# Performance work log

Measured on AMD Instinct MI355X. Metric: run time of the kernel, lower is better.

The kernel has to match this reference:

```python
import jax, jax.numpy as jnp
import numpy as np

VAR_W = 1.0
DIST_W = 1.0
M_VAR = 0.1
M_DIST = 1.5
IGNORE = 255
C = 16  # static upper bound on instance ids (labels 1..C; 0 = background)


def setup_inputs() -> dict:
    key = jax.random.key(0)
    ks = jax.random.split(key, 6)
    shapes = [(16, 1, 1024, 1024), (16, 1, 512, 512), (16, 1, 256, 256)]
    d = {}
    for idx, s in enumerate(shapes):
        d[f"featmap{idx}"] = jax.random.normal(ks[idx], s, dtype=jnp.float32)
        d[f"gt{idx}"] = jax.random.randint(ks[3 + idx], s, 0, C + 1, dtype=jnp.int32)
    return d


def _push_pull(feats, gts):
    B = feats[0].shape[0]
    nseg = B * (C + 1)
    b_off = (jnp.arange(B, dtype=jnp.int32) * (C + 1))[:, None]  # [B,1]

    segs, valids, ffs = [], [], []
    tot_sum = jnp.zeros((nseg,), dtype=feats[0].dtype)
    tot_cnt = jnp.zeros((nseg,), dtype=feats[0].dtype)
    # pass 1: per (batch, instance) sums / counts pooled over all scales
    for f, g in zip(feats, gts):
        ff = f.reshape(B, -1)            # [B, N_s]
        gg = g.reshape(B, -1)
        valid = (gg >= 1) & (gg <= C) & (gg < IGNORE)
        lab = jnp.where(valid, gg, 0)
        seg = (lab + b_off).reshape(-1)  # [B*N_s], segment id = b*(C+1)+label
        vf = valid.reshape(-1).astype(ff.dtype)
        tot_sum = tot_sum + jax.ops.segment_sum(jnp.where(valid, ff, 0.0).reshape(-1), seg, num_segments=nseg)
        tot_cnt = tot_cnt + jax.ops.segment_sum(vf, seg, num_segments=nseg)
        segs.append(seg); valids.append(valid); ffs.append(ff)

    mean = tot_sum / jnp.maximum(tot_cnt, 1.0)  # [nseg] per-(b,instance) mean over all scales

    # pass 2: pull loss -- per-scale mean of clamp(|x - mean| - margin_var, 0)^2, summed over scales
    pull_seg = jnp.zeros((nseg,), dtype=feats[0].dtype)
    for ff, seg, valid in zip(ffs, segs, valids):
        m_pix = mean[seg].reshape(ff.shape)
        val = jnp.where(valid, jnp.square(jnp.maximum(jnp.abs(ff - m_pix) - M_VAR, 0.0)), 0.0)
        ssum = jax.ops.segment_sum(val.reshape(-1), seg, num_segments=nseg)
        scnt = jax.ops.segment_sum(valid.reshape(-1).astype(ff.dtype), seg, num_segments=nseg)
        pull_seg = pull_seg + jnp.where(scnt > 0, ssum / jnp.maximum(scnt, 1.0), 0.0)

    present = tot_cnt.reshape(B, C + 1)[:, 1:] > 0        # [B,C]
    pull_i = pull_seg.reshape(B, C + 1)[:, 1:]            # [B,C]
    n_pull = jnp.maximum(present.sum(), 1).astype(pull_i.dtype)
    pull_loss = jnp.sum(jnp.where(present, pull_i, 0.0)) / n_pull * VAR_W

    # push loss: all ordered pairs (i,j), i!=j, both present in that batch element
    m = mean.reshape(B, C + 1)[:, 1:]                     # [B,C]
    diff = jnp.abs(m[:, :, None] - m[:, None, :])         # [B,C,C]
    pv = jnp.square(jnp.maximum(2.0 * M_DIST - diff, 0.0))
    pm = present[:, :, None] & present[:, None, :] & ~jnp.eye(C, dtype=bool)[None]
    n_push = jnp.maximum(pm.sum(), 1).astype(pv.dtype)
    push_loss = jnp.sum(jnp.where(pm, pv, 0.0)) / n_push * DIST_W

    return push_loss + pull_loss


def reference(featmap0, featmap1, featmap2, gt0, gt1, gt2):
    return _push_pull([featmap0, featmap1, featmap2], [gt0, gt1, gt2])
```

## Files before the change

kernel.cpp:

```cpp
#include <hip/hip_runtime.h>


#define M_VAR 0.1f
#define TWO_M_DIST 3.0f

#define SUB0 64
#define SUB1 16
#define SUB2 4
#define PER_BATCH (SUB0 + SUB1 + SUB2)
#define NBATCH 16
#define GRID_BLOCKS (NBATCH * PER_BATCH)
#define NITER 16

#define OFF_PSUM  0
#define OFF_PCNT  (GRID_BLOCKS * 16)
#define OFF_MI    (2 * GRID_BLOCKS * 16)
#define OFF_GMEAN (OFF_MI + 3 * 16 * 17 * 2)
#define OFF_GCNT  (OFF_GMEAN + 256)
#define OFF_PULL  (OFF_GCNT + 256)
#define OFF_PLAB  46592
#define PLAB_BASE1 (16 * 262144)
#define PLAB_BASE2 (PLAB_BASE1 + 16 * 65536)
#define PLAB_TOTAL (PLAB_BASE2 + 16 * 16384)
#define WS_NEEDED ((size_t)(OFF_PLAB + PLAB_TOTAL) * 4)

struct Sel {
  const float4* f; const int4* g;
  int vbase, stride, batch, j, pbase;
};

__device__ __forceinline__ Sel pick(
    int bid, int t,
    const float4* f0, const int4* g0,
    const float4* f1, const int4* g1,
    const float4* f2, const int4* g2) {
  Sel s;
  s.batch = bid / PER_BATCH;
  s.j = bid - s.batch * PER_BATCH;
  if (s.j < SUB0) {
    s.f = f0; s.g = g0; s.pbase = 0;
    s.vbase = s.batch * 262144 + s.j * 256 + t;             s.stride = SUB0 * 256;
  } else if (s.j < SUB0 + SUB1) {
    s.f = f1; s.g = g1; s.pbase = PLAB_BASE1; int sub = s.j - SUB0;
    s.vbase = s.batch * 65536 + sub * 256 + t;              s.stride = SUB1 * 256;
  } else {
    s.f = f2; s.g = g2; s.pbase = PLAB_BASE2; int sub = s.j - SUB0 - SUB1;
    s.vbase = s.batch * 16384 + sub * 256 + t;              s.stride = SUB2 * 256;
  }
  return s;
}

template <bool PACKED>
__global__ __launch_bounds__(256, 4) void hist_kernel(
    const float4* __restrict__ f0, const int4* __restrict__ g0,
    const float4* __restrict__ f1, const int4* __restrict__ g1,
    const float4* __restrict__ f2, const int4* __restrict__ g2,
    float* __restrict__ ws, unsigned* __restrict__ plab)
{
  const int t = threadIdx.x, bid = blockIdx.x;
  Sel s = pick(bid, t, f0, g0, f1, g1, f2, g2);

  float sum[16];
  int   cnt[16];
  #pragma unroll
  for (int l = 0; l < 16; ++l) { sum[l] = 0.f; cnt[l] = 0; }

  int v = s.vbase;
  float4 fA = s.f[v];            int4 gA = s.g[v];
  float4 fB = s.f[v + s.stride]; int4 gB = s.g[v + s.stride];

  #pragma unroll 1
  for (int it = 0; it < NITER; ++it) {
    int vp = (it + 2 < NITER) ? (v + 2 * s.stride) : v;
    float4 fC = s.f[vp];
    int4   gC = s.g[vp];

    #pragma unroll
    for (int l = 0; l < 16; ++l) {
      bool cx = (gA.x == l + 1); sum[l] += cx ? fA.x : 0.f; cnt[l] += cx;
      bool cy = (gA.y == l + 1); sum[l] += cy ? fA.y : 0.f; cnt[l] += cy;
      bool cz = (gA.z == l + 1); sum[l] += cz ? fA.z : 0.f; cnt[l] += cz;
      bool cw = (gA.w == l + 1); sum[l] += cw ? fA.w : 0.f; cnt[l] += cw;
    }
    if (PACKED) {
      unsigned lx = min((unsigned)gA.x, 16u), ly = min((unsigned)gA.y, 16u);
      unsigned lz = min((unsigned)gA.z, 16u), lw = min((unsigned)gA.w, 16u);
      plab[s.pbase + v] = lx | (ly << 8) | (lz << 16) | (lw << 24);
    }

    fA = fB; gA = gB; fB = fC; gB = gC;
    v += s.stride;
  }

  __shared__ float rs[4][16];
  __shared__ float rc[4][16];
  const int lane = t & 63, wave = t >> 6;
  #pragma unroll
  for (int l = 0; l < 16; ++l) {
    float sv = sum[l];
    float cv = (float)cnt[l];
    #pragma unroll
    for (int o = 32; o > 0; o >>= 1) {
      sv += __shfl_down(sv, o);
      cv += __shfl_down(cv, o);
    }
    if (lane == 0) { rs[wave][l] = sv; rc[wave][l] = cv; }
  }
  __syncthreads();
  if (t < 16) {
    ws[OFF_PSUM + bid * 16 + t] = rs[0][t] + rs[1][t] + rs[2][t] + rs[3][t];
    ws[OFF_PCNT + bid * 16 + t] = rc[0][t] + rc[1][t] + rc[2][t] + rc[3][t];
  }
}

__global__ __launch_bounds__(256) void mean_kernel(float* __restrict__ ws) {
  const int b = blockIdx.x;
  const int t = threadIdx.x;
  const int label = t & 15, k = t >> 4;

  float ts = 0.f, tc = 0.f, c0 = 0.f, c1 = 0.f, c2 = 0.f;
  for (int jj = k; jj < PER_BATCH; jj += 16) {
    float sv = ws[OFF_PSUM + (b * PER_BATCH + jj) * 16 + label];
    float cv = ws[OFF_PCNT + (b * PER_BATCH + jj) * 16 + label];
    ts += sv; tc += cv;
    if (jj < SUB0) c0 += cv; else if (jj < SUB0 + SUB1) c1 += cv; else c2 += cv;
  }
  __shared__ float L[5][16][16];
  L[0][k][label] = ts; L[1][k][label] = tc;
  L[2][k][label] = c0; L[3][k][label] = c1; L[4][k][label] = c2;
  __syncthreads();

  float2* mi = (float2*)(ws + OFF_MI);
  if (t < 16) {
    float Ts = 0.f, Tc = 0.f, C0 = 0.f, C1 = 0.f, C2 = 0.f;
    #pragma unroll 1
    for (int kk = 0; kk < 16; ++kk) {
      Ts += L[0][kk][t]; Tc += L[1][kk][t];
      C0 += L[2][kk][t]; C1 += L[3][kk][t]; C2 += L[4][kk][t];
    }
    float mean = Ts / fmaxf(Tc, 1.f);
    ws[OFF_GMEAN + b * 16 + t] = mean;
    ws[OFF_GCNT  + b * 16 + t] = Tc;
    mi[(0 * 16 + b) * 17 + 1 + t] = make_float2(mean, (C0 > 0.f) ? (1.f / C0) : 0.f);
    mi[(1 * 16 + b) * 17 + 1 + t] = make_float2(mean, (C1 > 0.f) ? (1.f / C1) : 0.f);
    mi[(2 * 16 + b) * 17 + 1 + t] = make_float2(mean, (C2 > 0.f) ? (1.f / C2) : 0.f);
  } else if (t == 16) {
    mi[(0 * 16 + b) * 17] = make_float2(0.f, 0.f);
    mi[(1 * 16 + b) * 17] = make_float2(0.f, 0.f);
    mi[(2 * 16 + b) * 17] = make_float2(0.f, 0.f);
  }
}

template <bool PACKED>
__global__ __launch_bounds__(256, 8) void pull_kernel(
    const float4* __restrict__ f0, const int4* __restrict__ g0,
    const float4* __restrict__ f1, const int4* __restrict__ g1,
    const float4* __restrict__ f2, const int4* __restrict__ g2,
    float* __restrict__ ws, const unsigned* __restrict__ plab)
{
  const int t = threadIdx.x, bid = blockIdx.x;
  Sel s = pick(bid, t, f0, g0, f1, g1, f2, g2);
  const int myscale = (s.j < SUB0) ? 0 : ((s.j < SUB0 + SUB1) ? 1 : 2);

  __shared__ float2 s_mi[17];
  if (t < 17) s_mi[t] = ((const float2*)(ws + OFF_MI))[(myscale * 16 + s.batch) * 17 + t];
  __syncthreads();

  float acc = 0.f;
  int v = s.vbase;
  if (PACKED) {
    float4  fA = s.f[v];               unsigned pA = plab[s.pbase + v];
    float4  fB = s.f[v + s.stride];    unsigned pB = plab[s.pbase + v + s.stride];
    #pragma unroll 1
    for (int it = 0; it < NITER; ++it) {
      int vp = (it + 2 < NITER) ? (v + 2 * s.stride) : v;
      float4  fC = s.f[vp];
      unsigned pC = plab[s.pbase + vp];
      {
        float2 a = s_mi[pA & 255u];
        float d = fmaxf(fabsf(fA.x - a.x) - M_VAR, 0.f); acc += d * d * a.y;
      }
      {
        float2 a = s_mi[(pA >> 8) & 255u];
        float d = fmaxf(fabsf(fA.y - a.x) - M_VAR, 0.f); acc += d * d * a.y;
      }
      {
        float2 a = s_mi[(pA >> 16) & 255u];
        float d = fmaxf(fabsf(fA.z - a.x) - M_VAR, 0.f); acc += d * d * a.y;
      }
      {
        float2 a = s_mi[pA >> 24];
        float d = fmaxf(fabsf(fA.w - a.x) - M_VAR, 0.f); acc += d * d * a.y;
      }
      fA = fB; pA = pB; fB = fC; pB = pC;
      v += s.stride;
    }
  } else {
    float4 fA = s.f[v];            int4 gA = s.g[v];
    float4 fB = s.f[v + s.stride]; int4 gB = s.g[v + s.stride];
    #pragma unroll 1
    for (int it = 0; it < NITER; ++it) {
      int vp = (it + 2 < NITER) ? (v + 2 * s.stride) : v;
      float4 fC = s.f[vp];
      int4   gC = s.g[vp];
      {
        float2 a = s_mi[min((unsigned)gA.x, 16u)];
        float d = fmaxf(fabsf(fA.x - a.x) - M_VAR, 0.f); acc += d * d * a.y;
      }
      {
        float2 a = s_mi[min((unsigned)gA.y, 16u)];
        float d = fmaxf(fabsf(fA.y - a.x) - M_VAR, 0.f); acc += d * d * a.y;
      }
      {
        float2 a = s_mi[min((unsigned)gA.z, 16u)];
        float d = fmaxf(fabsf(fA.z - a.x) - M_VAR, 0.f); acc += d * d * a.y;
      }
      {
        float2 a = s_mi[min((unsigned)gA.w, 16u)];
        float d = fmaxf(fabsf(fA.w - a.x) - M_VAR, 0.f); acc += d * d * a.y;
      }
      fA = fB; gA = gB; fB = fC; gB = gC;
      v += s.stride;
    }
  }

  #pragma unroll
  for (int o = 32; o > 0; o >>= 1) acc += __shfl_down(acc, o);
  __shared__ float racc[4];
  if ((t & 63) == 0) racc[t >> 6] = acc;
  __syncthreads();
  if (t == 0) ws[OFF_PULL + bid] = racc[0] + racc[1] + racc[2] + racc[3];
}

__global__ __launch_bounds__(256) void finalize_kernel(
    const float* __restrict__ ws, float* __restrict__ out)
{
  const int t = threadIdx.x;
  __shared__ float s_mean[256];
  __shared__ float s_pres[256];
  {
    float cval = ws[OFF_GCNT + t];
    s_mean[t] = ws[OFF_GMEAN + t];
    s_pres[t] = (cval > 0.f) ? 1.f : 0.f;
  }
  __syncthreads();

  float pull_v = 0.f;
  for (int i = t; i < GRID_BLOCKS; i += 256) pull_v += ws[OFF_PULL + i];

  float pull_n = s_pres[t];
  float push_v = 0.f, push_n = 0.f;
  {
    int b = t >> 4, ii = t & 15;
    if (s_pres[t] > 0.f) {
      float mi = s_mean[t];
      for (int jj = 0; jj < 16; ++jj) {
        if (jj == ii) continue;
        int sj = (b << 4) | jj;
        if (s_pres[sj] > 0.f) {
          float d = fmaxf(TWO_M_DIST - fabsf(mi - s_mean[sj]), 0.f);
          push_v += d * d; push_n += 1.f;
        }
      }
    }
  }

  #pragma unroll
  for (int o = 32; o > 0; o >>= 1) {
    pull_v += __shfl_down(pull_v, o);
    pull_n += __shfl_down(pull_n, o);
    push_v += __shfl_down(push_v, o);
    push_n += __shfl_down(push_n, o);
  }
  __shared__ float r[4][4];
  int wave = t >> 6;
  if ((t & 63) == 0) { r[wave][0] = pull_v; r[wave][1] = pull_n; r[wave][2] = push_v; r[wave][3] = push_n; }
  __syncthreads();
  if (t == 0) {
    float PV = 0, PN = 0, SV = 0, SN = 0;
    for (int w = 0; w < 4; ++w) { PV += r[w][0]; PN += r[w][1]; SV += r[w][2]; SN += r[w][3]; }
    out[0] = PV / fmaxf(PN, 1.f) + SV / fmaxf(SN, 1.f);
  }
}

extern "C" void kernel_launch(void* const* d_in, const int* in_sizes, int n_in,
                              void* d_out, int out_size, void* d_ws, size_t ws_size,
                              hipStream_t stream) {
  const float4* f0 = (const float4*)d_in[0];
  const int4*   g0 = (const int4*)  d_in[1];
  const float4* f1 = (const float4*)d_in[2];
  const int4*   g1 = (const int4*)  d_in[3];
  const float4* f2 = (const float4*)d_in[4];
  const int4*   g2 = (const int4*)  d_in[5];
  float*    ws   = (float*)d_ws;
  unsigned* plab = (unsigned*)d_ws + OFF_PLAB;
  float*    out  = (float*)d_out;

  const bool packed = (ws_size >= WS_NEEDED);
  if (packed) {
    hist_kernel<true><<<GRID_BLOCKS, 256, 0, stream>>>(f0, g0, f1, g1, f2, g2, ws, plab);
  } else {
    hist_kernel<false><<<GRID_BLOCKS, 256, 0, stream>>>(f0, g0, f1, g1, f2, g2, ws, plab);
  }
  mean_kernel<<<NBATCH, 256, 0, stream>>>(ws);
  if (packed) {
    pull_kernel<true><<<GRID_BLOCKS, 256, 0, stream>>>(f0, g0, f1, g1, f2, g2, ws, plab);
  } else {
    pull_kernel<false><<<GRID_BLOCKS, 256, 0, stream>>>(f0, g0, f1, g1, f2, g2, ws, plab);
  }
  finalize_kernel<<<1, 256, 0, stream>>>(ws, out);
}
```

Measured before the change: 227.3 us.

## Drop packed-label buffer, use two-level one-hot histogram with byte-packed counts

The histogram inner loop now splits each label into a high and low 2-bit index. It does 4+16 selects per pixel instead of 16 compare-accumulates, and keeps counts as 8-bit fields packed into four 32-bit registers. The packed-label side buffer is removed, so the pull pass rereads the raw int32 labels instead of writing and reading a compressed copy. The grid is doubled with contiguous 2048-element chunks and fewer iterations per block. Byte counters can hold at most 255 per thread, and each thread sees 32 pixels, so they are safe. Removing the packed buffer raises pull-pass traffic, which is meant to be offset by the cheaper histogram compute and lower write traffic.

```diff
diff --git a/kernel.cpp b/kernel.cpp
--- a/kernel.cpp
+++ b/kernel.cpp
@@ -4,13 +4,14 @@
 #define M_VAR 0.1f
 #define TWO_M_DIST 3.0f
 
-#define SUB0 64
-#define SUB1 16
-#define SUB2 4
-#define PER_BATCH (SUB0 + SUB1 + SUB2)
+#define NITER 8
+#define ELEMS 2048
+#define B0 128
+#define B1 32
+#define B2 8
+#define PER_BATCH (B0 + B1 + B2)
 #define NBATCH 16
 #define GRID_BLOCKS (NBATCH * PER_BATCH)
-#define NITER 16
 
 #define OFF_PSUM  0
 #define OFF_PCNT  (GRID_BLOCKS * 16)
@@ -18,15 +19,10 @@
 #define OFF_GMEAN (OFF_MI + 3 * 16 * 17 * 2)
 #define OFF_GCNT  (OFF_GMEAN + 256)
 #define OFF_PULL  (OFF_GCNT + 256)
-#define OFF_PLAB  46592
-#define PLAB_BASE1 (16 * 262144)
-#define PLAB_BASE2 (PLAB_BASE1 + 16 * 65536)
-#define PLAB_TOTAL (PLAB_BASE2 + 16 * 16384)
-#define WS_NEEDED ((size_t)(OFF_PLAB + PLAB_TOTAL) * 4)
 
 struct Sel {
   const float4* f; const int4* g;
-  int vbase, stride, batch, j, pbase;
+  int vbase, batch, j;
 };
 
 __device__ __forceinline__ Sel pick(
@@ -37,59 +33,77 @@
   Sel s;
   s.batch = bid / PER_BATCH;
   s.j = bid - s.batch * PER_BATCH;
-  if (s.j < SUB0) {
-    s.f = f0; s.g = g0; s.pbase = 0;
-    s.vbase = s.batch * 262144 + s.j * 256 + t;             s.stride = SUB0 * 256;
-  } else if (s.j < SUB0 + SUB1) {
-    s.f = f1; s.g = g1; s.pbase = PLAB_BASE1; int sub = s.j - SUB0;
-    s.vbase = s.batch * 65536 + sub * 256 + t;              s.stride = SUB1 * 256;
+  if (s.j < B0) {
+    s.f = f0; s.g = g0;
+    s.vbase = s.batch * 262144 + s.j * ELEMS + t;
+  } else if (s.j < B0 + B1) {
+    s.f = f1; s.g = g1;
+    s.vbase = s.batch * 65536 + (s.j - B0) * ELEMS + t;
   } else {
-    s.f = f2; s.g = g2; s.pbase = PLAB_BASE2; int sub = s.j - SUB0 - SUB1;
-    s.vbase = s.batch * 16384 + sub * 256 + t;              s.stride = SUB2 * 256;
+    s.f = f2; s.g = g2;
+    s.vbase = s.batch * 16384 + (s.j - B0 - B1) * ELEMS + t;
   }
   return s;
 }
 
-template <bool PACKED>
+__device__ __forceinline__ void hupd(float f, int g, float* __restrict__ sum,
+                                     unsigned* __restrict__ cp, unsigned one) {
+  unsigned lm = (unsigned)g - 1u;
+  unsigned hi = lm >> 2;
+  unsigned lo = lm & 3u;
+  float gf0 = (hi == 0u) ? f : 0.f;
+  float gf1 = (hi == 1u) ? f : 0.f;
+  float gf2 = (hi == 2u) ? f : 0.f;
+  float gf3 = (hi == 3u) ? f : 0.f;
+  unsigned inc = one << (lo << 3);
+  cp[0] += (hi == 0u) ? inc : 0u;
+  cp[1] += (hi == 1u) ? inc : 0u;
+  cp[2] += (hi == 2u) ? inc : 0u;
+  cp[3] += (hi == 3u) ? inc : 0u;
+  #pragma unroll
+  for (int c = 0; c < 4; ++c) {
+    bool mc = (lo == (unsigned)c);
+    sum[0 * 4 + c] += mc ? gf0 : 0.f;
+    sum[1 * 4 + c] += mc ? gf1 : 0.f;
+    sum[2 * 4 + c] += mc ? gf2 : 0.f;
+    sum[3 * 4 + c] += mc ? gf3 : 0.f;
+  }
+}
+
 __global__ __launch_bounds__(256, 4) void hist_kernel(
     const float4* __restrict__ f0, const int4* __restrict__ g0,
     const float4* __restrict__ f1, const int4* __restrict__ g1,
     const float4* __restrict__ f2, const int4* __restrict__ g2,
-    float* __restrict__ ws, unsigned* __restrict__ plab)
+    float* __restrict__ ws)
 {
   const int t = threadIdx.x, bid = blockIdx.x;
   Sel s = pick(bid, t, f0, g0, f1, g1, f2, g2);
 
   float sum[16];
-  int   cnt[16];
-  #pragma unroll
-  for (int l = 0; l < 16; ++l) { sum[l] = 0.f; cnt[l] = 0; }
+  unsigned cp[4];
+  #pragma unroll
+  for (int l = 0; l < 16; ++l) sum[l] = 0.f;
+  #pragma unroll
+  for (int r = 0; r < 4; ++r) cp[r] = 0u;
+  const unsigned one = 1u;
 
   int v = s.vbase;
-  float4 fA = s.f[v];            int4 gA = s.g[v];
-  float4 fB = s.f[v + s.stride]; int4 gB = s.g[v + s.stride];
+  float4 fA = s.f[v];        int4 gA = s.g[v];
+  float4 fB = s.f[v + 256];  int4 gB = s.g[v + 256];
 
   #pragma unroll 1
   for (int it = 0; it < NITER; ++it) {
-    int vp = (it + 2 < NITER) ? (v + 2 * s.stride) : v;
+    int vp = (it + 2 < NITER) ? (v + 512) : v;
     float4 fC = s.f[vp];
     int4   gC = s.g[vp];
 
-    #pragma unroll
-    for (int l = 0; l < 16; ++l) {
-      bool cx = (gA.x == l + 1); sum[l] += cx ? fA.x : 0.f; cnt[l] += cx;
-      bool cy = (gA.y == l + 1); sum[l] += cy ? fA.y : 0.f; cnt[l] += cy;
-      bool cz = (gA.z == l + 1); sum[l] += cz ? fA.z : 0.f; cnt[l] += cz;
-      bool cw = (gA.w == l + 1); sum[l] += cw ? fA.w : 0.f; cnt[l] += cw;
-    }
-    if (PACKED) {
-      unsigned lx = min((unsigned)gA.x, 16u), ly = min((unsigned)gA.y, 16u);
-      unsigned lz = min((unsigned)gA.z, 16u), lw = min((unsigned)gA.w, 16u);
-      plab[s.pbase + v] = lx | (ly << 8) | (lz << 16) | (lw << 24);
-    }
+    hupd(fA.x, gA.x, sum, cp, one);
+    hupd(fA.y, gA.y, sum, cp, one);
+    hupd(fA.z, gA.z, sum, cp, one);
+    hupd(fA.w, gA.w, sum, cp, one);
 
     fA = fB; gA = gB; fB = fC; gB = gC;
-    v += s.stride;
+    v += 256;
   }
 
   __shared__ float rs[4][16];
@@ -98,7 +112,7 @@
   #pragma unroll
   for (int l = 0; l < 16; ++l) {
     float sv = sum[l];
-    float cv = (float)cnt[l];
+    float cv = (float)((cp[l >> 2] >> ((l & 3) * 8)) & 255u);
     #pragma unroll
     for (int o = 32; o > 0; o >>= 1) {
       sv += __shfl_down(sv, o);
@@ -123,7 +137,7 @@
     float sv = ws[OFF_PSUM + (b * PER_BATCH + jj) * 16 + label];
     float cv = ws[OFF_PCNT + (b * PER_BATCH + jj) * 16 + label];
     ts += sv; tc += cv;
-    if (jj < SUB0) c0 += cv; else if (jj < SUB0 + SUB1) c1 += cv; else c2 += cv;
+    if (jj < B0) c0 += cv; else if (jj < B0 + B1) c1 += cv; else c2 += cv;
   }
   __shared__ float L[5][16][16];
   L[0][k][label] = ts; L[1][k][label] = tc;
@@ -151,16 +165,15 @@
   }
 }
 
-template <bool PACKED>
 __global__ __launch_bounds__(256, 8) void pull_kernel(
     const float4* __restrict__ f0, const int4* __restrict__ g0,
     const float4* __restrict__ f1, const int4* __restrict__ g1,
     const float4* __restrict__ f2, const int4* __restrict__ g2,
-    float* __restrict__ ws, const unsigned* __restrict__ plab)
+    float* __restrict__ ws)
 {
   const int t = threadIdx.x, bid = blockIdx.x;
   Sel s = pick(bid, t, f0, g0, f1, g1, f2, g2);
-  const int myscale = (s.j < SUB0) ? 0 : ((s.j < SUB0 + SUB1) ? 1 : 2);
+  const int myscale = (s.j < B0) ? 0 : ((s.j < B0 + B1) ? 1 : 2);
 
   __shared__ float2 s_mi[17];
   if (t < 17) s_mi[t] = ((const float2*)(ws + OFF_MI))[(myscale * 16 + s.batch) * 17 + t];
@@ -168,60 +181,32 @@
 
   float acc = 0.f;
   int v = s.vbase;
-  if (PACKED) {
-    float4  fA = s.f[v];               unsigned pA = plab[s.pbase + v];
-    float4  fB = s.f[v + s.stride];    unsigned pB = plab[s.pbase + v + s.stride];
-    #pragma unroll 1
-    for (int it = 0; it < NITER; ++it) {
-      int vp = (it + 2 < NITER) ? (v + 2 * s.stride) : v;
-      float4  fC = s.f[vp];
-      unsigned pC = plab[s.pbase + vp];
-      {
-        float2 a = s_mi[pA & 255u];
-        float d = fmaxf(fabsf(fA.x - a.x) - M_VAR, 0.f); acc += d * d * a.y;
-      }
-      {
-        float2 a = s_mi[(pA >> 8) & 255u];
-        float d = fmaxf(fabsf(fA.y - a.x) - M_VAR, 0.f); acc += d * d * a.y;
-      }
-      {
-        float2 a = s_mi[(pA >> 16) & 255u];
-        float d = fmaxf(fabsf(fA.z - a.x) - M_VAR, 0.f); acc += d * d * a.y;
-      }
-      {
-        float2 a = s_mi[pA >> 24];
-        float d = fmaxf(fabsf(fA.w - a.x) - M_VAR, 0.f); acc += d * d * a.y;
-      }
-      fA = fB; pA = pB; fB = fC; pB = pC;
-      v += s.stride;
-    }
-  } else {
-    float4 fA = s.f[v];            int4 gA = s.g[v];
-    float4 fB = s.f[v + s.stride]; int4 gB = s.g[v + s.stride];
-    #pragma unroll 1
-    for (int it = 0; it < NITER; ++it) {
-      int vp = (it + 2 < NITER) ? (v + 2 * s.stride) : v;
-      float4 fC = s.f[vp];
-      int4   gC = s.g[vp];
-      {
-        float2 a = s_mi[min((unsigned)gA.x, 16u)];
-        float d = fmaxf(fabsf(fA.x - a.x) - M_VAR, 0.f); acc += d * d * a.y;
-      }
-      {
-        float2 a = s_mi[min((unsigned)gA.y, 16u)];
-        float d = fmaxf(fabsf(fA.y - a.x) - M_VAR, 0.f); acc += d * d * a.y;
-      }
-      {
-        float2 a = s_mi[min((unsigned)gA.z, 16u)];
-        float d = fmaxf(fabsf(fA.z - a.x) - M_VAR, 0.f); acc += d * d * a.y;
-      }
-      {
-        float2 a = s_mi[min((unsigned)gA.w, 16u)];
-        float d = fmaxf(fabsf(fA.w - a.x) - M_VAR, 0.f); acc += d * d * a.y;
-      }
-      fA = fB; gA = gB; fB = fC; gB = gC;
-      v += s.stride;
-    }
+  float4 fA = s.f[v];        int4 gA = s.g[v];
+  float4 fB = s.f[v + 256];  int4 gB = s.g[v + 256];
+
+  #pragma unroll 1
+  for (int it = 0; it < NITER; ++it) {
+    int vp = (it + 2 < NITER) ? (v + 512) : v;
+    float4 fC = s.f[vp];
+    int4   gC = s.g[vp];
+    {
+      float2 a = s_mi[min((unsigned)gA.x, 16u)];
+      float d = fmaxf(fabsf(fA.x - a.x) - M_VAR, 0.f); acc += d * d * a.y;
+    }
+    {
+      float2 a = s_mi[min((unsigned)gA.y, 16u)];
+      float d = fmaxf(fabsf(fA.y - a.x) - M_VAR, 0.f); acc += d * d * a.y;
+    }
+    {
+      float2 a = s_mi[min((unsigned)gA.z, 16u)];
+      float d = fmaxf(fabsf(fA.z - a.x) - M_VAR, 0.f); acc += d * d * a.y;
+    }
+    {
+      float2 a = s_mi[min((unsigned)gA.w, 16u)];
+      float d = fmaxf(fabsf(fA.w - a.x) - M_VAR, 0.f); acc += d * d * a.y;
+    }
+    fA = fB; gA = gB; fB = fC; gB = gC;
+    v += 256;
   }
 
   #pragma unroll
@@ -292,21 +277,11 @@
   const int4*   g1 = (const int4*)  d_in[3];
   const float4* f2 = (const float4*)d_in[4];
   const int4*   g2 = (const int4*)  d_in[5];
-  float*    ws   = (float*)d_ws;
-  unsigned* plab = (unsigned*)d_ws + OFF_PLAB;
-  float*    out  = (float*)d_out;
-
-  const bool packed = (ws_size >= WS_NEEDED);
-  if (packed) {
-    hist_kernel<true><<<GRID_BLOCKS, 256, 0, stream>>>(f0, g0, f1, g1, f2, g2, ws, plab);
-  } else {
-    hist_kernel<false><<<GRID_BLOCKS, 256, 0, stream>>>(f0, g0, f1, g1, f2, g2, ws, plab);
-  }
+  float* ws  = (float*)d_ws;
+  float* out = (float*)d_out;
+
+  hist_kernel<<<GRID_BLOCKS, 256, 0, stream>>>(f0, g0, f1, g1, f2, g2, ws);
   mean_kernel<<<NBATCH, 256, 0, stream>>>(ws);
-  if (packed) {
-    pull_kernel<true><<<GRID_BLOCKS, 256, 0, stream>>>(f0, g0, f1, g1, f2, g2, ws, plab);
-  } else {
-    pull_kernel<false><<<GRID_BLOCKS, 256, 0, stream>>>(f0, g0, f1, g1, f2, g2, ws, plab);
-  }
+  pull_kernel<<<GRID_BLOCKS, 256, 0, stream>>>(f0, g0, f1, g1, f2, g2, ws);
   finalize_kernel<<<1, 256, 0, stream>>>(ws, out);
 }
```

After: 220.0 us. 3.2% less time.
